# Kernel optimization log

Hardware: AMD Instinct MI355X
Metric: run time of the kernel (lower is better)

The kernel has to match this reference:

```python
import jax, jax.numpy as jnp
import numpy as np

N = 50000
E = 600000
IN_CH = 128
HID = 64


def setup_inputs() -> dict:
    key = jax.random.key(0)
    ks = jax.random.split(key, 8)
    x = jax.random.normal(ks[0], (N, IN_CH), dtype=jnp.float32)
    edge_index = jax.random.randint(ks[1], (2, E), 0, N, dtype=jnp.int64)
    s = 1.0 / np.sqrt(IN_CH)
    W_rel = jax.random.uniform(ks[2], (IN_CH, HID), jnp.float32, -s, s)
    b_rel = jax.random.uniform(ks[3], (HID,), jnp.float32, -s, s)
    W_root = jax.random.uniform(ks[4], (IN_CH, HID), jnp.float32, -s, s)
    sh = 1.0 / np.sqrt(HID)
    W_dec = jax.random.uniform(ks[5], (HID, IN_CH), jnp.float32, -sh, sh)
    b_dec = jax.random.uniform(ks[6], (IN_CH,), jnp.float32, -sh, sh)
    return {"x": x, "edge_index": edge_index, "W_rel": W_rel, "b_rel": b_rel,
            "W_root": W_root, "W_dec": W_dec, "b_dec": b_dec}


def reference(x, edge_index, W_rel, b_rel, W_root, W_dec, b_dec):
    src, dst = edge_index[0], edge_index[1]
    # gather source node features, sum-aggregate at destination nodes  [N, IN_CH]
    agg = jax.ops.segment_sum(x[src], dst, num_segments=N)
    # GraphConv: lin_rel(agg) + lin_root(x)  (lin_rel carries the bias)
    h = agg @ W_rel + b_rel + x @ W_root
    h = jax.nn.relu(h)
    # linear decoder back to input feature space
    return h @ W_dec + b_dec
```

## Files before the change

kernel.cpp:

```cpp
#include <hip/hip_runtime.h>

#define IN_CH 128
#define HID 64
#define ELLW 32
#define SPILLCAP 4096
#define NSCAT 256
#define BCAP 3584

typedef short v8s __attribute__((ext_vector_type(8)));
typedef float v4f __attribute__((ext_vector_type(4)));

__device__ __forceinline__ unsigned int bf16pair(float a, float b) {
    unsigned int ua = __float_as_uint(a);
    unsigned int ub = __float_as_uint(b);
    ua = (ua + 0x7fffu + ((ua >> 16) & 1u)) >> 16;
    ub = (ub + 0x7fffu + ((ub >> 16) & 1u)) & 0xffff0000u;
    return ua | ub;
}
__device__ __forceinline__ unsigned short bf16of(float a) {
    unsigned int ua = __float_as_uint(a);
    return (unsigned short)((ua + 0x7fffu + ((ua >> 16) & 1u)) >> 16);
}

__global__ __launch_bounds__(256) void graphmae_prep(
    const float* __restrict__ W_rel, const float* __restrict__ W_root,
    const float* __restrict__ W_dec,
    unsigned short* __restrict__ Bt, unsigned short* __restrict__ Wdt,
    int* __restrict__ bucketcur, int NZ)
{
    const int idx = blockIdx.x * 256 + threadIdx.x;
    if (idx < NZ) bucketcur[idx] = 0;
    if (idx < 16384) {
        const int k = idx >> 7;
        const int c = idx & 127;
        const float v = (c < HID) ? W_rel[(size_t)k * HID + c]
                                  : W_root[(size_t)k * HID + (c - HID)];
        Bt[(size_t)c * 128 + k] = bf16of(v);
    } else if (idx < 24576) {
        const int j = idx - 16384;
        const int k = j >> 7;
        const int c = j & 127;
        Wdt[(size_t)c * 64 + k] = bf16of(W_dec[(size_t)k * IN_CH + c]);
    }
}

__global__ __launch_bounds__(512) void graphmae_encode_scatter(
    const float* __restrict__ x, const unsigned short* __restrict__ Bt,
    const float* __restrict__ b_rel, const int* __restrict__ ei,
    unsigned short* __restrict__ y16, float* __restrict__ agg,
    int* __restrict__ bucketcur, unsigned int* __restrict__ sorted,
    int* __restrict__ spillcnt, int2* __restrict__ spill,
    int N, int E, int NBUK, int CE)
{
    __shared__ int lh[256];
    __shared__ int lcur[256];

    const int t  = threadIdx.x;
    const int n0 = blockIdx.x * 64;
    const bool sduty = (blockIdx.x < NSCAT);
    const int e0 = blockIdx.x * CE;
    const int e1 = sduty ? min(E, e0 + CE) : 0;

    if (t >= 256) { lh[t - 256] = 0; lcur[t - 256] = 0; }
    __syncthreads();

    if (t < 256) {
        const int w    = t >> 6;
        const int lane = t & 63;
        const int mr   = lane & 15;
        const int kg   = lane >> 4;
        const int nrow = n0 + w * 16 + mr;

        v8s xfrag[4];
        #pragma unroll
        for (int ks = 0; ks < 4; ++ks) {
            uint4 pk = make_uint4(0u, 0u, 0u, 0u);
            if (nrow < N) {
                const float* xp = x + (size_t)nrow * IN_CH + ks * 32 + kg * 8;
                const float4 u0 = *(const float4*)(xp);
                const float4 u1 = *(const float4*)(xp + 4);
                pk = make_uint4(bf16pair(u0.x, u0.y), bf16pair(u0.z, u0.w),
                                bf16pair(u1.x, u1.y), bf16pair(u1.z, u1.w));
            }
            xfrag[ks] = *(v8s*)&pk;
        }

        #pragma unroll
        for (int ct = 0; ct < 8; ++ct) {
            v4f acc = {0.f, 0.f, 0.f, 0.f};
            const unsigned short* bp = Bt + (size_t)(ct * 16 + mr) * 128 + kg * 8;
            #pragma unroll
            for (int ks = 0; ks < 4; ++ks) {
                const v8s b = *(const v8s*)(bp + ks * 32);
                acc = __builtin_amdgcn_mfma_f32_16x16x32_bf16(b, xfrag[ks], acc, 0, 0, 0);
            }
            if (nrow < N) {
                if (ct < 4) {
                    const int c = ct * 16 + kg * 4;
                    *(uint2*)(y16 + (size_t)nrow * HID + c) =
                        make_uint2(bf16pair(acc[0], acc[1]), bf16pair(acc[2], acc[3]));
                } else {
                    const int c = (ct - 4) * 16 + kg * 4;
                    const float4 br = *(const float4*)(b_rel + c);
                    *(float4*)(agg + (size_t)nrow * HID + c) =
                        make_float4(acc[0] + br.x, acc[1] + br.y,
                                    acc[2] + br.z, acc[3] + br.w);
                }
            }
        }
    } else if (sduty) {
        for (int e = e0 + (t - 256); e < e1; e += 256)
            atomicAdd(&lh[ei[E + e] >> 8], 1);
    }
    __syncthreads();

    if (t >= 256 && sduty) {
        const int b = t - 256;
        if (b < NBUK) {
            const int cnt = lh[b];
            if (cnt > 0) lcur[b] = atomicAdd(&bucketcur[b], cnt);
        }
    }
    __syncthreads();

    if (t >= 256 && sduty) {
        for (int e = e0 + (t - 256); e < e1; e += 256) {
            const int d = ei[E + e];
            const int s = ei[e];
            const int b = d >> 8;
            const int pos = atomicAdd(&lcur[b], 1);
            if (pos < BCAP) {
                sorted[(size_t)b * BCAP + pos] =
                    ((unsigned)(d & 255) << 16) | (unsigned)s;
            } else {
                const int p = atomicAdd(spillcnt, 1);
                if (p < SPILLCAP) spill[p] = make_int2(d, s);
            }
        }
    }
}

__global__ __launch_bounds__(256) void bucket_fill(
    const unsigned int* __restrict__ sorted, const int* __restrict__ bucketcur,
    int* __restrict__ deg, unsigned short* __restrict__ slots16,
    int* __restrict__ spillcnt, int2* __restrict__ spill)
{
    __shared__ int cnt[256];
    __shared__ unsigned short sl[256 * ELLW];
    const int t = threadIdx.x, b = blockIdx.x;
    cnt[t] = 0;
    __syncthreads();

    const int m = min(bucketcur[b], BCAP);
    const unsigned int* src = sorted + (size_t)b * BCAP;
    for (int i = t; i < m; i += 256) {
        const unsigned int v = src[i];
        const int dl = v >> 16;
        const int r = atomicAdd(&cnt[dl], 1);
        if (r < ELLW) sl[dl * ELLW + r] = (unsigned short)(v & 0xffffu);
        else {
            const int p = atomicAdd(spillcnt, 1);
            if (p < SPILLCAP) spill[p] = make_int2((b << 8) + dl, (int)(v & 0xffffu));
        }
    }
    __syncthreads();

    deg[(b << 8) + t] = cnt[t];
    unsigned int* g = (unsigned int*)slots16 + (size_t)b * 4096;
    const unsigned int* l = (const unsigned int*)sl;
    for (int i = t; i < 4096; i += 256) g[i] = l[i];
}

__global__ __launch_bounds__(256) void graphmae_gather(
    const int* __restrict__ deg, const unsigned short* __restrict__ slots16,
    const unsigned short* __restrict__ y16, const float* __restrict__ agg,
    const int* __restrict__ spillcnt, const int2* __restrict__ spill,
    unsigned short* __restrict__ h16, int N)
{
    const int n = blockIdx.x * 4 + (threadIdx.x >> 6);
    if (n >= N) return;
    const int lane = threadIdx.x & 63;
    const int es   = lane >> 3;
    const int cl   = lane & 7;

    const int cnt = min(deg[n], ELLW);
    const unsigned short* sp = slots16 + (size_t)n * ELLW;

    float4 a0 = make_float4(0.f, 0.f, 0.f, 0.f);
    float4 a1 = make_float4(0.f, 0.f, 0.f, 0.f);
    if (es == 0) {
        a0 = *(const float4*)(agg + (size_t)n * HID + cl * 8);
        a1 = *(const float4*)(agg + (size_t)n * HID + cl * 8 + 4);
    }

    float acc[8];
    #pragma unroll
    for (int j = 0; j < 8; ++j) acc[j] = 0.f;

    for (int e = es; e < cnt; e += 8) {
        const int s = sp[e];
        const uint4 v = *(const uint4*)(y16 + (size_t)s * HID + cl * 8);
        acc[0] += __uint_as_float(v.x << 16);
        acc[1] += __uint_as_float(v.x & 0xffff0000u);
        acc[2] += __uint_as_float(v.y << 16);
        acc[3] += __uint_as_float(v.y & 0xffff0000u);
        acc[4] += __uint_as_float(v.z << 16);
        acc[5] += __uint_as_float(v.z & 0xffff0000u);
        acc[6] += __uint_as_float(v.w << 16);
        acc[7] += __uint_as_float(v.w & 0xffff0000u);
    }

    const int spN = min(*spillcnt, SPILLCAP);
    for (int i = es; i < spN; i += 8) {
        const int2 e2 = spill[i];
        if (e2.x == n) {
            const uint4 v = *(const uint4*)(y16 + (size_t)e2.y * HID + cl * 8);
            acc[0] += __uint_as_float(v.x << 16);
            acc[1] += __uint_as_float(v.x & 0xffff0000u);
            acc[2] += __uint_as_float(v.y << 16);
            acc[3] += __uint_as_float(v.y & 0xffff0000u);
            acc[4] += __uint_as_float(v.z << 16);
            acc[5] += __uint_as_float(v.z & 0xffff0000u);
            acc[6] += __uint_as_float(v.w << 16);
            acc[7] += __uint_as_float(v.w & 0xffff0000u);
        }
    }

    #pragma unroll
    for (int m = 8; m <= 32; m <<= 1) {
        #pragma unroll
        for (int j = 0; j < 8; ++j) acc[j] += __shfl_xor(acc[j], m);
    }

    if (es == 0) {
        const float h0 = fmaxf(a0.x + acc[0], 0.f);
        const float h1 = fmaxf(a0.y + acc[1], 0.f);
        const float h2 = fmaxf(a0.z + acc[2], 0.f);
        const float h3 = fmaxf(a0.w + acc[3], 0.f);
        const float h4 = fmaxf(a1.x + acc[4], 0.f);
        const float h5 = fmaxf(a1.y + acc[5], 0.f);
        const float h6 = fmaxf(a1.z + acc[6], 0.f);
        const float h7 = fmaxf(a1.w + acc[7], 0.f);
        uint4 o;
        o.x = bf16pair(h0, h1);
        o.y = bf16pair(h2, h3);
        o.z = bf16pair(h4, h5);
        o.w = bf16pair(h6, h7);
        *(uint4*)(h16 + (size_t)n * HID + cl * 8) = o;
    }
}

__global__ __launch_bounds__(256) void graphmae_decode(
    const unsigned short* __restrict__ h16, const unsigned short* __restrict__ Wdt,
    const float* __restrict__ b_dec, float* __restrict__ out, int N)
{
    const int t  = threadIdx.x;
    const int n0 = blockIdx.x * 64;
    const int w    = t >> 6;
    const int lane = t & 63;
    const int mr   = lane & 15;
    const int kg   = lane >> 4;
    const int nrow = n0 + w * 16 + mr;

    v8s hfrag[2];
    #pragma unroll
    for (int ks = 0; ks < 2; ++ks) {
        uint4 pk = make_uint4(0u, 0u, 0u, 0u);
        if (nrow < N)
            pk = *(const uint4*)(h16 + (size_t)nrow * HID + ks * 32 + kg * 8);
        hfrag[ks] = *(v8s*)&pk;
    }

    #pragma unroll
    for (int ct = 0; ct < 8; ++ct) {
        v4f acc = {0.f, 0.f, 0.f, 0.f};
        const unsigned short* wp = Wdt + (size_t)(ct * 16 + mr) * 64 + kg * 8;
        #pragma unroll
        for (int ks = 0; ks < 2; ++ks) {
            const v8s b = *(const v8s*)(wp + ks * 32);
            acc = __builtin_amdgcn_mfma_f32_16x16x32_bf16(b, hfrag[ks], acc, 0, 0, 0);
        }
        if (nrow < N) {
            const int c = ct * 16 + kg * 4;
            const float4 bd = *(const float4*)(b_dec + c);
            *(float4*)(out + (size_t)nrow * IN_CH + c) =
                make_float4(acc[0] + bd.x, acc[1] + bd.y,
                            acc[2] + bd.z, acc[3] + bd.w);
        }
    }
}

extern "C" void kernel_launch(void* const* d_in, const int* in_sizes, int n_in,
                              void* d_out, int out_size, void* d_ws, size_t ws_size,
                              hipStream_t stream)
{
    const float* x      = (const float*)d_in[0];
    const int*   ei     = (const int*)  d_in[1];
    const float* W_rel  = (const float*)d_in[2];
    const float* b_rel  = (const float*)d_in[3];
    const float* W_root = (const float*)d_in[4];
    const float* W_dec  = (const float*)d_in[5];
    const float* b_dec  = (const float*)d_in[6];
    float* out = (float*)d_out;

    const int N = in_sizes[0] / IN_CH;
    const int E = in_sizes[1] / 2;

    const int NBUK = (N + 255) / 256;
    const int NPAD = NBUK * 256;
    const int CE   = (E + NSCAT - 1) / NSCAT;

    unsigned short* y16 = (unsigned short*)d_ws;
    float* agg          = (float*)(y16 + (size_t)N * HID);
    unsigned short* h16 = (unsigned short*)(agg + (size_t)N * HID);
    int* deg            = (int*)(h16 + (size_t)N * HID);
    unsigned short* slots16 = (unsigned short*)(deg + NPAD);
    unsigned int* sorted = (unsigned int*)(slots16 + (size_t)NPAD * ELLW);
    int* bucketcur = (int*)(sorted + (size_t)NBUK * BCAP);
    int* spillcnt  = bucketcur + NBUK;
    int2* spill    = (int2*)(spillcnt + 3);
    unsigned short* Bt  = (unsigned short*)(spill + SPILLCAP);
    unsigned short* Wdt = Bt + 128 * 128;

    const int nblk64 = (N + 63) / 64;

    graphmae_prep<<<96, 256, 0, stream>>>(W_rel, W_root, W_dec, Bt, Wdt,
                                          bucketcur, NBUK + 1);

    graphmae_encode_scatter<<<nblk64, 512, 0, stream>>>(
        x, Bt, b_rel, ei, y16, agg,
        bucketcur, sorted, spillcnt, spill, N, E, NBUK, CE);

    bucket_fill<<<NBUK, 256, 0, stream>>>(sorted, bucketcur, deg, slots16,
                                          spillcnt, spill);

    const int gblk = (N + 3) / 4;
    graphmae_gather<<<gblk, 256, 0, stream>>>(deg, slots16, y16, agg,
                                              spillcnt, spill, h16, N);
    graphmae_decode<<<nblk64, 256, 0, stream>>>(h16, Wdt, b_dec, out, N);
}
```

Measured before the change: 81.87 us.

## Fuse bucket fill and neighbor gather into one kernel using shared-memory ELL slots

Merges the bucket_fill and gather kernels. Each block now takes a 32-node slice of a 256-node bucket, builds the ELL neighbor lists for that slice in shared memory, and gathers y16 rows straight from there. Overflow edges go to a small shared local spill list. This removes the global deg/slots16 round trip and one kernel launch. The cost is that each of the 8 blocks per bucket rescans the whole bucket's sorted edge list, and each wave now handles 8 nodes one after another instead of one node each.

```diff
diff --git a/kernel.cpp b/kernel.cpp
--- a/kernel.cpp
+++ b/kernel.cpp
@@ -4,6 +4,7 @@
 #define HID 64
 #define ELLW 32
 #define SPILLCAP 4096
+#define LSPCAP 128
 #define NSCAT 256
 #define BCAP 3584
 
@@ -140,81 +141,71 @@
     }
 }
 
-__global__ __launch_bounds__(256) void bucket_fill(
+__global__ __launch_bounds__(256) void bucket_gather(
     const unsigned int* __restrict__ sorted, const int* __restrict__ bucketcur,
-    int* __restrict__ deg, unsigned short* __restrict__ slots16,
-    int* __restrict__ spillcnt, int2* __restrict__ spill)
-{
-    __shared__ int cnt[256];
-    __shared__ unsigned short sl[256 * ELLW];
-    const int t = threadIdx.x, b = blockIdx.x;
-    cnt[t] = 0;
+    const unsigned short* __restrict__ y16, const float* __restrict__ agg,
+    const int* __restrict__ spillcnt, const int2* __restrict__ spill,
+    unsigned short* __restrict__ h16, int N)
+{
+    __shared__ unsigned short sl[32 * ELLW];
+    __shared__ int cnt[32];
+    __shared__ int lsp[LSPCAP];
+    __shared__ int lspcnt;
+
+    const int t   = threadIdx.x;
+    const int b   = blockIdx.x >> 3;
+    const int spl = blockIdx.x & 7;
+    const int dlo = spl * 32;
+
+    if (t < 32) cnt[t] = 0;
+    if (t == 32) lspcnt = 0;
     __syncthreads();
 
     const int m = min(bucketcur[b], BCAP);
     const unsigned int* src = sorted + (size_t)b * BCAP;
     for (int i = t; i < m; i += 256) {
         const unsigned int v = src[i];
-        const int dl = v >> 16;
-        const int r = atomicAdd(&cnt[dl], 1);
-        if (r < ELLW) sl[dl * ELLW + r] = (unsigned short)(v & 0xffffu);
-        else {
-            const int p = atomicAdd(spillcnt, 1);
-            if (p < SPILLCAP) spill[p] = make_int2((b << 8) + dl, (int)(v & 0xffffu));
-        }
-    }
-    __syncthreads();
-
-    deg[(b << 8) + t] = cnt[t];
-    unsigned int* g = (unsigned int*)slots16 + (size_t)b * 4096;
-    const unsigned int* l = (const unsigned int*)sl;
-    for (int i = t; i < 4096; i += 256) g[i] = l[i];
-}
-
-__global__ __launch_bounds__(256) void graphmae_gather(
-    const int* __restrict__ deg, const unsigned short* __restrict__ slots16,
-    const unsigned short* __restrict__ y16, const float* __restrict__ agg,
-    const int* __restrict__ spillcnt, const int2* __restrict__ spill,
-    unsigned short* __restrict__ h16, int N)
-{
-    const int n = blockIdx.x * 4 + (threadIdx.x >> 6);
-    if (n >= N) return;
-    const int lane = threadIdx.x & 63;
+        const int dl = (int)(v >> 16) - dlo;
+        if ((unsigned)dl < 32u) {
+            const int r = atomicAdd(&cnt[dl], 1);
+            if (r < ELLW) {
+                sl[dl * ELLW + r] = (unsigned short)(v & 0xffffu);
+            } else {
+                const int p = atomicAdd(&lspcnt, 1);
+                if (p < LSPCAP) lsp[p] = (dl << 16) | (int)(v & 0xffffu);
+            }
+        }
+    }
+    __syncthreads();
+
+    const int wid  = t >> 6;
+    const int lane = t & 63;
     const int es   = lane >> 3;
     const int cl   = lane & 7;
-
-    const int cnt = min(deg[n], ELLW);
-    const unsigned short* sp = slots16 + (size_t)n * ELLW;
-
-    float4 a0 = make_float4(0.f, 0.f, 0.f, 0.f);
-    float4 a1 = make_float4(0.f, 0.f, 0.f, 0.f);
-    if (es == 0) {
-        a0 = *(const float4*)(agg + (size_t)n * HID + cl * 8);
-        a1 = *(const float4*)(agg + (size_t)n * HID + cl * 8 + 4);
-    }
-
-    float acc[8];
-    #pragma unroll
-    for (int j = 0; j < 8; ++j) acc[j] = 0.f;
-
-    for (int e = es; e < cnt; e += 8) {
-        const int s = sp[e];
-        const uint4 v = *(const uint4*)(y16 + (size_t)s * HID + cl * 8);
-        acc[0] += __uint_as_float(v.x << 16);
-        acc[1] += __uint_as_float(v.x & 0xffff0000u);
-        acc[2] += __uint_as_float(v.y << 16);
-        acc[3] += __uint_as_float(v.y & 0xffff0000u);
-        acc[4] += __uint_as_float(v.z << 16);
-        acc[5] += __uint_as_float(v.z & 0xffff0000u);
-        acc[6] += __uint_as_float(v.w << 16);
-        acc[7] += __uint_as_float(v.w & 0xffff0000u);
-    }
-
-    const int spN = min(*spillcnt, SPILLCAP);
-    for (int i = es; i < spN; i += 8) {
-        const int2 e2 = spill[i];
-        if (e2.x == n) {
-            const uint4 v = *(const uint4*)(y16 + (size_t)e2.y * HID + cl * 8);
+    const int lspN = min(lspcnt, LSPCAP);
+    const int spN  = min(*spillcnt, SPILLCAP);
+
+    for (int j = 0; j < 8; ++j) {
+        const int dl = wid * 8 + j;
+        const int n  = (b << 8) + dlo + dl;
+        if (n >= N) continue;
+        const int c_ = min(cnt[dl], ELLW);
+        const unsigned short* sp = sl + dl * ELLW;
+
+        float4 a0 = make_float4(0.f, 0.f, 0.f, 0.f);
+        float4 a1 = make_float4(0.f, 0.f, 0.f, 0.f);
+        if (es == 0) {
+            a0 = *(const float4*)(agg + (size_t)n * HID + cl * 8);
+            a1 = *(const float4*)(agg + (size_t)n * HID + cl * 8 + 4);
+        }
+
+        float acc[8];
+        #pragma unroll
+        for (int q = 0; q < 8; ++q) acc[q] = 0.f;
+
+        for (int e = es; e < c_; e += 8) {
+            const int s = sp[e];
+            const uint4 v = *(const uint4*)(y16 + (size_t)s * HID + cl * 8);
             acc[0] += __uint_as_float(v.x << 16);
             acc[1] += __uint_as_float(v.x & 0xffff0000u);
             acc[2] += __uint_as_float(v.y << 16);
@@ -224,29 +215,58 @@
             acc[6] += __uint_as_float(v.w << 16);
             acc[7] += __uint_as_float(v.w & 0xffff0000u);
         }
-    }
-
-    #pragma unroll
-    for (int m = 8; m <= 32; m <<= 1) {
-        #pragma unroll
-        for (int j = 0; j < 8; ++j) acc[j] += __shfl_xor(acc[j], m);
-    }
-
-    if (es == 0) {
-        const float h0 = fmaxf(a0.x + acc[0], 0.f);
-        const float h1 = fmaxf(a0.y + acc[1], 0.f);
-        const float h2 = fmaxf(a0.z + acc[2], 0.f);
-        const float h3 = fmaxf(a0.w + acc[3], 0.f);
-        const float h4 = fmaxf(a1.x + acc[4], 0.f);
-        const float h5 = fmaxf(a1.y + acc[5], 0.f);
-        const float h6 = fmaxf(a1.z + acc[6], 0.f);
-        const float h7 = fmaxf(a1.w + acc[7], 0.f);
-        uint4 o;
-        o.x = bf16pair(h0, h1);
-        o.y = bf16pair(h2, h3);
-        o.z = bf16pair(h4, h5);
-        o.w = bf16pair(h6, h7);
-        *(uint4*)(h16 + (size_t)n * HID + cl * 8) = o;
+        for (int i = es; i < lspN; i += 8) {
+            const int e2 = lsp[i];
+            if ((e2 >> 16) == dl) {
+                const int s = e2 & 0xffff;
+                const uint4 v = *(const uint4*)(y16 + (size_t)s * HID + cl * 8);
+                acc[0] += __uint_as_float(v.x << 16);
+                acc[1] += __uint_as_float(v.x & 0xffff0000u);
+                acc[2] += __uint_as_float(v.y << 16);
+                acc[3] += __uint_as_float(v.y & 0xffff0000u);
+                acc[4] += __uint_as_float(v.z << 16);
+                acc[5] += __uint_as_float(v.z & 0xffff0000u);
+                acc[6] += __uint_as_float(v.w << 16);
+                acc[7] += __uint_as_float(v.w & 0xffff0000u);
+            }
+        }
+        for (int i = es; i < spN; i += 8) {
+            const int2 e2 = spill[i];
+            if (e2.x == n) {
+                const uint4 v = *(const uint4*)(y16 + (size_t)e2.y * HID + cl * 8);
+                acc[0] += __uint_as_float(v.x << 16);
+                acc[1] += __uint_as_float(v.x & 0xffff0000u);
+                acc[2] += __uint_as_float(v.y << 16);
+                acc[3] += __uint_as_float(v.y & 0xffff0000u);
+                acc[4] += __uint_as_float(v.z << 16);
+                acc[5] += __uint_as_float(v.z & 0xffff0000u);
+                acc[6] += __uint_as_float(v.w << 16);
+                acc[7] += __uint_as_float(v.w & 0xffff0000u);
+            }
+        }
+
+        #pragma unroll
+        for (int mk = 8; mk <= 32; mk <<= 1) {
+            #pragma unroll
+            for (int q = 0; q < 8; ++q) acc[q] += __shfl_xor(acc[q], mk);
+        }
+
+        if (es == 0) {
+            const float h0 = fmaxf(a0.x + acc[0], 0.f);
+            const float h1 = fmaxf(a0.y + acc[1], 0.f);
+            const float h2 = fmaxf(a0.z + acc[2], 0.f);
+            const float h3 = fmaxf(a0.w + acc[3], 0.f);
+            const float h4 = fmaxf(a1.x + acc[4], 0.f);
+            const float h5 = fmaxf(a1.y + acc[5], 0.f);
+            const float h6 = fmaxf(a1.z + acc[6], 0.f);
+            const float h7 = fmaxf(a1.w + acc[7], 0.f);
+            uint4 o;
+            o.x = bf16pair(h0, h1);
+            o.y = bf16pair(h2, h3);
+            o.z = bf16pair(h4, h5);
+            o.w = bf16pair(h6, h7);
+            *(uint4*)(h16 + (size_t)n * HID + cl * 8) = o;
+        }
     }
 }
 
@@ -307,15 +327,12 @@
     const int E = in_sizes[1] / 2;
 
     const int NBUK = (N + 255) / 256;
-    const int NPAD = NBUK * 256;
     const int CE   = (E + NSCAT - 1) / NSCAT;
 
     unsigned short* y16 = (unsigned short*)d_ws;
     float* agg          = (float*)(y16 + (size_t)N * HID);
     unsigned short* h16 = (unsigned short*)(agg + (size_t)N * HID);
-    int* deg            = (int*)(h16 + (size_t)N * HID);
-    unsigned short* slots16 = (unsigned short*)(deg + NPAD);
-    unsigned int* sorted = (unsigned int*)(slots16 + (size_t)NPAD * ELLW);
+    unsigned int* sorted = (unsigned int*)(h16 + (size_t)N * HID);
     int* bucketcur = (int*)(sorted + (size_t)NBUK * BCAP);
     int* spillcnt  = bucketcur + NBUK;
     int2* spill    = (int2*)(spillcnt + 3);
@@ -331,11 +348,8 @@
         x, Bt, b_rel, ei, y16, agg,
         bucketcur, sorted, spillcnt, spill, N, E, NBUK, CE);
 
-    bucket_fill<<<NBUK, 256, 0, stream>>>(sorted, bucketcur, deg, slots16,
-                                          spillcnt, spill);
-
-    const int gblk = (N + 3) / 4;
-    graphmae_gather<<<gblk, 256, 0, stream>>>(deg, slots16, y16, agg,
-                                              spillcnt, spill, h16, N);
+    bucket_gather<<<NBUK * 8, 256, 0, stream>>>(sorted, bucketcur, y16, agg,
+                                                spillcnt, spill, h16, N);
+
     graphmae_decode<<<nblk64, 256, 0, stream>>>(h16, Wdt, b_dec, out, N);
 }
```

Result: faster. 80.16 us (-2.1%).
